# Optimization experiments

Hardware: AMD Instinct MI355X
Metric: run time of the kernel (lower is better)

## Reference

```python
import jax, jax.numpy as jnp
import numpy as np


def setup_inputs() -> dict:
    key = jax.random.key(0)
    k1, k2, k3 = jax.random.split(key, 3)
    n_nodes, d = 1_000_000, 128
    B, L, w, neg_size = 1024, 80, 5, 4
    A = L - w + 1  # 76 anchors per walk
    walk = jax.random.randint(k1, (B, L), 0, n_nodes)
    # torch.randint(low=1, high=n_nodes-1) -> values in [1, n_nodes-2]
    neg = jax.random.randint(k2, (B, A, neg_size), 1, n_nodes - 1)
    embed = jax.random.normal(k3, (n_nodes, d), dtype=jnp.float32)
    return {"walk": walk, "neg": neg, "embed": embed}


def reference(walk, neg, embed):
    B, L = walk.shape
    A = neg.shape[1]          # L - window_size + 1
    w = L - A + 1             # window_size
    anc = walk[:, :A]                                       # [B, A]
    # pos[b, t, i] = walk[b, t + 1 + i], i in [0, w-2]
    sl = jnp.arange(A)[:, None] + jnp.arange(1, w)[None, :]  # [A, w-1]
    pos = walk[:, sl]                                        # [B, A, w-1]
    e_anc = embed[anc]                                       # [B, A, D]
    # fused gather + per-window dot products
    pos_logit = jnp.einsum('bacd,bad->bac', embed[pos], e_anc)  # [B, A, w-1]
    neg_logit = jnp.einsum('bacd,bad->bac', embed[neg], e_anc)  # [B, A, neg]
    # BCEWithLogitsLoss with labels 1 (pos) and 0 (neg), mean over all elements:
    #   label=1 -> softplus(-x);  label=0 -> softplus(x)
    total = pos_logit.size + neg_logit.size
    loss = (jnp.sum(jax.nn.softplus(-pos_logit)) +
            jnp.sum(jax.nn.softplus(neg_logit))) / total
    return loss
```

## Files before the change

### kernel.cpp

```cpp
#include <hip/hip_runtime.h>
#include <math.h>

#define BD   1024
#define LW   80
#define AA   76
#define NEGS 4
#define D    128
#define PAIRS (BD * AA)
#define WAVES_PER_BLOCK 4
#define PAIRS_PER_WAVE 19
#define NBLOCKS BD

__device__ __forceinline__ float softplus(float x) {
    return fmaxf(x, 0.0f) + log1pf(__expf(-fabsf(x)));
}

__device__ __forceinline__ float dot4(float4 a, float4 b) {
    return fmaf(a.x, b.x, fmaf(a.y, b.y, fmaf(a.z, b.z, a.w * b.w)));
}

__device__ __forceinline__ float4 sel4(bool c, float4 a, float4 b) {
    float4 r;
    r.x = c ? a.x : b.x;  r.y = c ? a.y : b.y;
    r.z = c ? a.z : b.z;  r.w = c ? a.w : b.w;
    return r;
}

__device__ __forceinline__ float4 swap32(float4 v) {
    float4 r;
    r.x = __shfl_xor(v.x, 32);  r.y = __shfl_xor(v.y, 32);
    r.z = __shfl_xor(v.z, 32);  r.w = __shfl_xor(v.w, 32);
    return r;
}

__device__ __forceinline__ float4 pload(const float* ebase, bool half, int i0, int i1) {
    const int idx = half ? i1 : i0;
    return *(const float4*)(ebase + (size_t)idx * D);
}

__global__ __launch_bounds__(256, 4) void sg_partial(
    const int* __restrict__ walk, const int* __restrict__ neg,
    const float* __restrict__ embed, float* __restrict__ ws)
{
    __shared__ float s_wsum[WAVES_PER_BLOCK];
    const int tid  = threadIdx.x;
    const int lane = tid & 63;
    const int l32  = lane & 31;
    const bool half = lane >= 32;
    const int wave = __builtin_amdgcn_readfirstlane(tid >> 6);
    const int b    = blockIdx.x;
    const int a0   = wave * PAIRS_PER_WAVE;

    const float* ebase = embed + l32 * 4;
    const int*   wrow  = walk + b * LW + a0;
    const int*   nrow  = neg + (size_t)(b * AA + a0) * NEGS;

    float4 w01 = pload(ebase, half, wrow[0], wrow[1]);
    float4 w23 = pload(ebase, half, wrow[2], wrow[3]);
    float4 w45 = pload(ebase, half, wrow[4], wrow[5]);

    int4 nva = *(const int4*)(nrow);
    int4 nvb = *(const int4*)(nrow + 4);
    float4 n01 = pload(ebase, half, nva.x, nva.y);
    float4 n23 = pload(ebase, half, nva.z, nva.w);
    float4 n45 = pload(ebase, half, nvb.x, nvb.y);
    float4 n67 = pload(ebase, half, nvb.z, nvb.w);

    const bool hi1 = lane & 1;
    const bool hi2 = lane & 2;
    const bool hi3 = lane & 4;

    float wsum = 0.0f;
    float tsum = 0.0f;

    #pragma unroll
    for (int d = 0; d < 9; ++d) {
        float4 nw, m01, m23, m45, m67;
        if (d < 8) {
            nw = pload(ebase, half, wrow[2*d + 6], wrow[2*d + 7]);
            const int4 pa = *(const int4*)(nrow + 8*(d + 1));
            const int4 pb = *(const int4*)(nrow + 8*(d + 1) + 4);
            m01 = pload(ebase, half, pa.x, pa.y);
            m23 = pload(ebase, half, pa.z, pa.w);
            m45 = pload(ebase, half, pb.x, pb.y);
            m67 = pload(ebase, half, pb.z, pb.w);
        } else {
            const int i22 = wrow[22];
            nw = pload(ebase, half, i22, i22);
            const int4 pa = *(const int4*)(nrow + 72);
            m01 = pload(ebase, half, pa.x, pa.y);
            m23 = pload(ebase, half, pa.z, pa.w);
            m45 = m01;  m67 = m23;
        }

        const float4 Y   = swap32(w01);
        const float4 Z0  = sel4(half, Y, w01);
        const float4 Z1  = sel4(half, w01, Y);
        const float4 Aop = sel4(half, w01, w23);
        const float4 Bop = sel4(half, w23, w45);

        const float a0v = dot4(Z0, Aop);
        const float a1v = dot4(Z0, Bop);
        const float a2v = dot4(Z1, w23);
        const float a3v = dot4(Z1, w45);
        const float a4v = dot4(Z0, n01);
        const float a5v = dot4(Z0, n23);
        const float a6v = dot4(Z1, n45);
        const float a7v = dot4(Z1, n67);

        float b0 = (hi1 ? a4v : a0v) + __shfl_xor(hi1 ? a0v : a4v, 1);
        float b1 = (hi1 ? a5v : a1v) + __shfl_xor(hi1 ? a1v : a5v, 1);
        float b2 = (hi1 ? a6v : a2v) + __shfl_xor(hi1 ? a2v : a6v, 1);
        float b3 = (hi1 ? a7v : a3v) + __shfl_xor(hi1 ? a3v : a7v, 1);

        float c0 = (hi2 ? b2 : b0) + __shfl_xor(hi2 ? b0 : b2, 2);
        float c1 = (hi2 ? b3 : b1) + __shfl_xor(hi2 ? b1 : b3, 2);

        float dv = (hi3 ? c1 : c0) + __shfl_xor(hi3 ? c0 : c1, 4);
        dv += __shfl_xor(dv, 8);
        dv += __shfl_xor(dv, 16);
        wsum += softplus(hi1 ? dv : -dv);

        w01 = w23;  w23 = w45;  w45 = nw;
        n01 = m01;  n23 = m23;  n45 = m45;  n67 = m67;
    }

    {
        const float4 Y   = swap32(w01);
        const float4 Z0  = sel4(half, Y, w01);
        const float4 Aop = sel4(half, w01, w23);
        const float4 Bop = sel4(half, w23, w45);

        const float t0 = dot4(Z0, Aop);
        const float t1 = dot4(Z0, Bop);
        const float t2 = dot4(Z0, n01);
        const float t3 = dot4(Z0, n23);

        float u0 = (hi1 ? t2 : t0) + __shfl_xor(hi1 ? t0 : t2, 1);
        float u1 = (hi1 ? t3 : t1) + __shfl_xor(hi1 ? t1 : t3, 1);
        float v  = (hi2 ? u1 : u0) + __shfl_xor(hi2 ? u0 : u1, 2);
        v += __shfl_xor(v, 4);
        v += __shfl_xor(v, 8);
        v += __shfl_xor(v, 16);
        tsum = softplus(hi1 ? v : -v);
    }

    float tot = wsum + 0.5f * tsum;
    #pragma unroll
    for (int m = 1; m < 64; m <<= 1) tot += __shfl_xor(tot, m);

    if (lane == 0) s_wsum[wave] = tot * 0.25f;
    __syncthreads();
    if (tid == 0)
        ws[blockIdx.x] = s_wsum[0] + s_wsum[1] + s_wsum[2] + s_wsum[3];
}

__global__ __launch_bounds__(256) void sg_reduce(
    const float* __restrict__ ws, float* __restrict__ out)
{
    __shared__ float s[4];
    const int tid = threadIdx.x;
    float sum = 0.0f;
    #pragma unroll
    for (int i = 0; i < NBLOCKS / 256; ++i) sum += ws[tid + i * 256];
    #pragma unroll
    for (int m = 1; m < 64; m <<= 1) sum += __shfl_xor(sum, m);
    const int wave = tid >> 6;
    const int lane = tid & 63;
    if (lane == 0) s[wave] = sum;
    __syncthreads();
    if (tid == 0) {
        const float total = (float)((size_t)PAIRS * 8);
        out[0] = (s[0] + s[1] + s[2] + s[3]) * (1.0f / total);
    }
}

extern "C" void kernel_launch(void* const* d_in, const int* in_sizes, int n_in,
                              void* d_out, int out_size, void* d_ws, size_t ws_size,
                              hipStream_t stream) {
    const int*   walk  = (const int*)d_in[0];
    const int*   neg   = (const int*)d_in[1];
    const float* embed = (const float*)d_in[2];
    float* ws  = (float*)d_ws;
    float* out = (float*)d_out;

    sg_partial<<<NBLOCKS, 256, 0, stream>>>(walk, neg, embed, ws);
    sg_reduce<<<1, 256, 0, stream>>>(ws, out);
}
```

Measured before the change: 586.5 us.

## Split each 19-anchor chunk across two waves with 128-thread blocks

Each walk is now handled by four blocks of two waves instead of one block of four waves. Within a block, one wave processes the first 10 anchors and the other wave the remaining 9 anchors plus the tail anchor. This doubles the number of waves and halves the serial dependent gather chain per wave, to expose more memory-level parallelism for the random embedding loads. The cost is extra block overhead and partial sums, plus some redundant loads of overlapping window rows at the wave boundary.

```diff
diff --git a/kernel.cpp b/kernel.cpp
--- a/kernel.cpp
+++ b/kernel.cpp
@@ -7,9 +7,8 @@
 #define NEGS 4
 #define D    128
 #define PAIRS (BD * AA)
-#define WAVES_PER_BLOCK 4
-#define PAIRS_PER_WAVE 19
-#define NBLOCKS BD
+#define CHUNKS 4
+#define NBLOCKS (BD * CHUNKS)
 
 __device__ __forceinline__ float softplus(float x) {
     return fmaxf(x, 0.0f) + log1pf(__expf(-fabsf(x)));
@@ -38,34 +37,24 @@
     return *(const float4*)(ebase + (size_t)idx * D);
 }
 
-__global__ __launch_bounds__(256, 4) void sg_partial(
+__global__ __launch_bounds__(128, 6) void sg_partial(
     const int* __restrict__ walk, const int* __restrict__ neg,
     const float* __restrict__ embed, float* __restrict__ ws)
 {
-    __shared__ float s_wsum[WAVES_PER_BLOCK];
+    __shared__ float s_wsum[2];
     const int tid  = threadIdx.x;
     const int lane = tid & 63;
     const int l32  = lane & 31;
     const bool half = lane >= 32;
     const int wave = __builtin_amdgcn_readfirstlane(tid >> 6);
-    const int b    = blockIdx.x;
-    const int a0   = wave * PAIRS_PER_WAVE;
+    const int b     = blockIdx.x >> 2;
+    const int chunk = blockIdx.x & 3;
+    const int a0    = chunk * 19;
 
     const float* ebase = embed + l32 * 4;
     const int*   wrow  = walk + b * LW + a0;
     const int*   nrow  = neg + (size_t)(b * AA + a0) * NEGS;
 
-    float4 w01 = pload(ebase, half, wrow[0], wrow[1]);
-    float4 w23 = pload(ebase, half, wrow[2], wrow[3]);
-    float4 w45 = pload(ebase, half, wrow[4], wrow[5]);
-
-    int4 nva = *(const int4*)(nrow);
-    int4 nvb = *(const int4*)(nrow + 4);
-    float4 n01 = pload(ebase, half, nva.x, nva.y);
-    float4 n23 = pload(ebase, half, nva.z, nva.w);
-    float4 n45 = pload(ebase, half, nvb.x, nvb.y);
-    float4 n67 = pload(ebase, half, nvb.z, nvb.w);
-
     const bool hi1 = lane & 1;
     const bool hi2 = lane & 2;
     const bool hi3 = lane & 4;
@@ -73,26 +62,8 @@
     float wsum = 0.0f;
     float tsum = 0.0f;
 
-    #pragma unroll
-    for (int d = 0; d < 9; ++d) {
-        float4 nw, m01, m23, m45, m67;
-        if (d < 8) {
-            nw = pload(ebase, half, wrow[2*d + 6], wrow[2*d + 7]);
-            const int4 pa = *(const int4*)(nrow + 8*(d + 1));
-            const int4 pb = *(const int4*)(nrow + 8*(d + 1) + 4);
-            m01 = pload(ebase, half, pa.x, pa.y);
-            m23 = pload(ebase, half, pa.z, pa.w);
-            m45 = pload(ebase, half, pb.x, pb.y);
-            m67 = pload(ebase, half, pb.z, pb.w);
-        } else {
-            const int i22 = wrow[22];
-            nw = pload(ebase, half, i22, i22);
-            const int4 pa = *(const int4*)(nrow + 72);
-            m01 = pload(ebase, half, pa.x, pa.y);
-            m23 = pload(ebase, half, pa.z, pa.w);
-            m45 = m01;  m67 = m23;
-        }
-
+    auto dstep = [&](float4 w01, float4 w23, float4 w45,
+                     float4 n01, float4 n23, float4 n45, float4 n67) {
         const float4 Y   = swap32(w01);
         const float4 Z0  = sel4(half, Y, w01);
         const float4 Z1  = sel4(half, w01, Y);
@@ -120,29 +91,93 @@
         dv += __shfl_xor(dv, 8);
         dv += __shfl_xor(dv, 16);
         wsum += softplus(hi1 ? dv : -dv);
-
-        w01 = w23;  w23 = w45;  w45 = nw;
-        n01 = m01;  n23 = m23;  n45 = m45;  n67 = m67;
-    }
-
-    {
-        const float4 Y   = swap32(w01);
-        const float4 Z0  = sel4(half, Y, w01);
-        const float4 Aop = sel4(half, w01, w23);
-        const float4 Bop = sel4(half, w23, w45);
-
-        const float t0 = dot4(Z0, Aop);
-        const float t1 = dot4(Z0, Bop);
-        const float t2 = dot4(Z0, n01);
-        const float t3 = dot4(Z0, n23);
-
-        float u0 = (hi1 ? t2 : t0) + __shfl_xor(hi1 ? t0 : t2, 1);
-        float u1 = (hi1 ? t3 : t1) + __shfl_xor(hi1 ? t1 : t3, 1);
-        float v  = (hi2 ? u1 : u0) + __shfl_xor(hi2 ? u0 : u1, 2);
-        v += __shfl_xor(v, 4);
-        v += __shfl_xor(v, 8);
-        v += __shfl_xor(v, 16);
-        tsum = softplus(hi1 ? v : -v);
+    };
+
+    if (wave == 0) {
+        float4 w01 = pload(ebase, half, wrow[0], wrow[1]);
+        float4 w23 = pload(ebase, half, wrow[2], wrow[3]);
+        float4 w45 = pload(ebase, half, wrow[4], wrow[5]);
+        const int4 nva = *(const int4*)(nrow);
+        const int4 nvb = *(const int4*)(nrow + 4);
+        float4 n01 = pload(ebase, half, nva.x, nva.y);
+        float4 n23 = pload(ebase, half, nva.z, nva.w);
+        float4 n45 = pload(ebase, half, nvb.x, nvb.y);
+        float4 n67 = pload(ebase, half, nvb.z, nvb.w);
+
+        #pragma unroll
+        for (int d = 0; d < 5; ++d) {
+            float4 nw, m01, m23, m45, m67;
+            if (d < 4) {
+                nw = pload(ebase, half, wrow[2*d + 6], wrow[2*d + 7]);
+                const int4 pa = *(const int4*)(nrow + 8*(d + 1));
+                const int4 pb = *(const int4*)(nrow + 8*(d + 1) + 4);
+                m01 = pload(ebase, half, pa.x, pa.y);
+                m23 = pload(ebase, half, pa.z, pa.w);
+                m45 = pload(ebase, half, pb.x, pb.y);
+                m67 = pload(ebase, half, pb.z, pb.w);
+            }
+            dstep(w01, w23, w45, n01, n23, n45, n67);
+            if (d < 4) {
+                w01 = w23;  w23 = w45;  w45 = nw;
+                n01 = m01;  n23 = m23;  n45 = m45;  n67 = m67;
+            }
+        }
+    } else {
+        const int* wr = wrow + 10;
+        const int* nr = nrow + 40;
+        float4 w01 = pload(ebase, half, wr[0], wr[1]);
+        float4 w23 = pload(ebase, half, wr[2], wr[3]);
+        float4 w45 = pload(ebase, half, wr[4], wr[5]);
+        const int4 nva = *(const int4*)(nr);
+        const int4 nvb = *(const int4*)(nr + 4);
+        float4 n01 = pload(ebase, half, nva.x, nva.y);
+        float4 n23 = pload(ebase, half, nva.z, nva.w);
+        float4 n45 = pload(ebase, half, nvb.x, nvb.y);
+        float4 n67 = pload(ebase, half, nvb.z, nvb.w);
+
+        #pragma unroll
+        for (int d = 0; d < 4; ++d) {
+            float4 nw, m01, m23, m45, m67;
+            if (d < 3) {
+                nw = pload(ebase, half, wr[2*d + 6], wr[2*d + 7]);
+                const int4 pa = *(const int4*)(nr + 8*(d + 1));
+                const int4 pb = *(const int4*)(nr + 8*(d + 1) + 4);
+                m01 = pload(ebase, half, pa.x, pa.y);
+                m23 = pload(ebase, half, pa.z, pa.w);
+                m45 = pload(ebase, half, pb.x, pb.y);
+                m67 = pload(ebase, half, pb.z, pb.w);
+            } else {
+                const int i22 = wr[12];
+                nw = pload(ebase, half, i22, i22);
+                const int4 pa = *(const int4*)(nr + 32);
+                m01 = pload(ebase, half, pa.x, pa.y);
+                m23 = pload(ebase, half, pa.z, pa.w);
+                m45 = m01;  m67 = m23;
+            }
+            dstep(w01, w23, w45, n01, n23, n45, n67);
+            w01 = w23;  w23 = w45;  w45 = nw;
+            n01 = m01;  n23 = m23;  n45 = m45;  n67 = m67;
+        }
+
+        {
+            const float4 Y   = swap32(w01);
+            const float4 Z0  = sel4(half, Y, w01);
+            const float4 Aop = sel4(half, w01, w23);
+            const float4 Bop = sel4(half, w23, w45);
+
+            const float t0 = dot4(Z0, Aop);
+            const float t1 = dot4(Z0, Bop);
+            const float t2 = dot4(Z0, n01);
+            const float t3 = dot4(Z0, n23);
+
+            float u0 = (hi1 ? t2 : t0) + __shfl_xor(hi1 ? t0 : t2, 1);
+            float u1 = (hi1 ? t3 : t1) + __shfl_xor(hi1 ? t1 : t3, 1);
+            float v  = (hi2 ? u1 : u0) + __shfl_xor(hi2 ? u0 : u1, 2);
+            v += __shfl_xor(v, 4);
+            v += __shfl_xor(v, 8);
+            v += __shfl_xor(v, 16);
+            tsum = softplus(hi1 ? v : -v);
+        }
     }
 
     float tot = wsum + 0.5f * tsum;
@@ -152,7 +187,7 @@
     if (lane == 0) s_wsum[wave] = tot * 0.25f;
     __syncthreads();
     if (tid == 0)
-        ws[blockIdx.x] = s_wsum[0] + s_wsum[1] + s_wsum[2] + s_wsum[3];
+        ws[blockIdx.x] = s_wsum[0] + s_wsum[1];
 }
 
 __global__ __launch_bounds__(256) void sg_reduce(
@@ -184,6 +219,6 @@
     float* ws  = (float*)d_ws;
     float* out = (float*)d_out;
 
-    sg_partial<<<NBLOCKS, 256, 0, stream>>>(walk, neg, embed, ws);
+    sg_partial<<<NBLOCKS, 128, 0, stream>>>(walk, neg, embed, ws);
     sg_reduce<<<1, 256, 0, stream>>>(ws, out);
 }
```

Result: no change. 588.0 us (+0.3%).
